# Kernel optimization log

Measured on AMD Instinct MI355X. Metric: run time of the kernel, lower is better.

The kernel has to match this reference:

```python
import jax, jax.numpy as jnp
import numpy as np


def setup_inputs() -> dict:
    key = jax.random.key(0)
    ks = jax.random.split(key, 8)
    b, l, d_model = 2, 2048, 1024
    d_inner, d_state, dt_rank, d_conv = 2048, 16, 64, 4
    g = lambda k, shape, s: jax.random.normal(k, shape, jnp.float32) * s
    A = jnp.broadcast_to(jnp.arange(1, d_state + 1, dtype=jnp.float32), (d_inner, d_state))
    return {
        "x": g(ks[0], (b, l, d_model), 1.0),
        "W_in": g(ks[1], (d_model, 2 * d_inner), 0.02),
        "W_conv": g(ks[2], (d_inner, 1, d_conv), 0.1),
        "b_conv": g(ks[3], (d_inner,), 0.1),
        "W_x": g(ks[4], (d_inner, dt_rank + 2 * d_state), 0.02),
        "W_dt": g(ks[5], (dt_rank, d_inner), 0.02),
        "b_dt": g(ks[6], (d_inner,), 0.1),
        "A_log": jnp.log(A),
        "D": jnp.ones((d_inner,), jnp.float32),
        "W_out": g(ks[7], (d_inner, d_model), 0.02),
    }


def _selective_scan(x, delta, A, B, C, D):
    # x, delta: (b, l, d); A: (d, n); B, C: (b, l, n); D: (d,)
    b, l, d = x.shape
    n = A.shape[1]

    def step(h, inp):
        dt, Bt, Ct, xt = inp  # (b,d), (b,n), (b,n), (b,d)
        dA = jnp.exp(dt[:, :, None] * A)                     # (b,d,n)
        h = dA * h + (dt * xt)[:, :, None] * Bt[:, None, :]  # (b,d,n)
        y = jnp.einsum('bdn,bn->bd', h, Ct)
        return h, y

    h0 = jnp.zeros((b, d, n), x.dtype)
    xs = (jnp.swapaxes(delta, 0, 1), jnp.swapaxes(B, 0, 1),
          jnp.swapaxes(C, 0, 1), jnp.swapaxes(x, 0, 1))
    _, ys = jax.lax.scan(step, h0, xs)   # ys: (l, b, d)
    return jnp.swapaxes(ys, 0, 1) + D * x


def _mamba(x, W_in, W_conv, b_conv, W_x, W_dt, b_dt, A_log, D, W_out):
    b, l, _ = x.shape
    d_inner = W_conv.shape[0]
    d_conv = W_conv.shape[2]
    dt_rank = W_dt.shape[0]
    n = A_log.shape[1]

    xr = x @ W_in                                   # (b,l,2*d_inner)
    xin, res = xr[..., :d_inner], xr[..., d_inner:]

    # depthwise causal conv1d (left pad d_conv-1 == torch pad both + trim to l)
    xc = jnp.swapaxes(xin, 1, 2)                    # (b,d_inner,l)
    xc = jax.lax.conv_general_dilated(
        xc, W_conv, window_strides=(1,), padding=[(d_conv - 1, 0)],
        feature_group_count=d_inner,
        dimension_numbers=('NCH', 'OIH', 'NCH')) + b_conv[None, :, None]
    xs = jax.nn.silu(jnp.swapaxes(xc, 1, 2))        # (b,l,d_inner)

    x_dbl = xs @ W_x                                # (b,l,dt_rank+2n)
    delta = jax.nn.softplus(x_dbl[..., :dt_rank] @ W_dt + b_dt)
    Bm = x_dbl[..., dt_rank:dt_rank + n]
    Cm = x_dbl[..., dt_rank + n:]
    A = -jnp.exp(A_log)

    y = _selective_scan(xs, delta, A, Bm, Cm, D)
    y = y * jax.nn.silu(res)
    return y @ W_out


def reference(x, W_in, W_conv, b_conv, W_x, W_dt, b_dt, A_log, D, W_out):
    return _mamba(x, W_in, W_conv, b_conv, W_x, W_dt, b_dt, A_log, D, W_out)
```

## Files before the change

### kernel.cpp

```cpp
#include <hip/hip_runtime.h>


typedef unsigned short ushort_t;
using short8 = __attribute__((ext_vector_type(8))) short;
using f32x4  = __attribute__((ext_vector_type(4))) float;
using gptr_t = const __attribute__((address_space(1))) unsigned short*;
using sptr_t = __attribute__((address_space(3))) unsigned short*;

#define NC 64
#define CL 32

__device__ inline ushort_t f2bf(float v) {
    unsigned u = __float_as_uint(v);
    unsigned r = (u + 0x7fff + ((u >> 16) & 1)) >> 16;
    return (ushort_t)r;
}
__device__ inline float bf2f(ushort_t h) { return __uint_as_float(((unsigned)h) << 16); }
__device__ inline void split2(float v, ushort_t& h, ushort_t& l) {
    h = f2bf(v);
    l = f2bf(v - bf2f(h));
}

__global__ __launch_bounds__(256) void convert_all(
    const float* __restrict__ x, ushort_t* __restrict__ xh, ushort_t* __restrict__ xl,
    const float* __restrict__ W_in, ushort_t* __restrict__ winh, ushort_t* __restrict__ winl,
    const float* __restrict__ W_out, ushort_t* __restrict__ wouth, ushort_t* __restrict__ woutl,
    const float* __restrict__ W_x, ushort_t* __restrict__ wxh, ushort_t* __restrict__ wxl) {
    __shared__ float tile[32][33];
    const int id = blockIdx.x;
    if (id < 4096) {
        int i = id * 256 + threadIdx.x;
        float4 v = ((const float4*)x)[i];
        ushort4 hh, ll;
        split2(v.x, hh.x, ll.x); split2(v.y, hh.y, ll.y);
        split2(v.z, hh.z, ll.z); split2(v.w, hh.w, ll.w);
        ((ushort4*)xh)[i] = hh;
        ((ushort4*)xl)[i] = ll;
        return;
    }
    const float* W; ushort_t *Th, *Tl; int K, N, bx, by;
    if (id < 8192)       { W = W_in;  Th = winh;  Tl = winl;  K = 1024; N = 4096;
                           bx = (id - 4096) & 127; by = (id - 4096) >> 7; }
    else if (id < 10240) { W = W_out; Th = wouth; Tl = woutl; K = 2048; N = 1024;
                           bx = (id - 8192) & 31;  by = (id - 8192) >> 5; }
    else                 { W = W_x;   Th = wxh;   Tl = wxl;   K = 2048; N = 96;
                           bx = (id - 10240) & 3;  by = (id - 10240) >> 2; }
    int n0 = bx * 32, k0 = by * 32;
    int tx = threadIdx.x & 31, ty = threadIdx.x >> 5;
    #pragma unroll
    for (int j = 0; j < 4; ++j) {
        int k = ty + j * 8;
        tile[k][tx] = (n0 + tx < N) ? W[(size_t)(k0 + k) * N + n0 + tx] : 0.f;
    }
    __syncthreads();
    #pragma unroll
    for (int j = 0; j < 4; ++j) {
        int nrow = ty + j * 8;
        float v = tile[tx][nrow];
        ushort_t h, l;
        split2(v, h, l);
        size_t o = (size_t)(n0 + nrow) * K + k0 + tx;
        Th[o] = h; Tl[o] = l;
    }
}

__global__ __launch_bounds__(512, 2) void gemm_mfma3_256(
    const ushort_t* __restrict__ Ah, const ushort_t* __restrict__ Al,
    const ushort_t* __restrict__ Bh, const ushort_t* __restrict__ Bl,
    float* __restrict__ C, int M, int N, int K, int ksteps, int partial_stride) {
    __shared__ ushort_t lds[65536];
    const int tid  = threadIdx.x;
    const int w    = tid >> 6;
    const int lane = tid & 63;
    const int wr = w >> 2;
    const int wc = w & 3;
    const int fr = lane & 15;
    const int kq = (lane >> 4) * 8;
    const int bm = blockIdx.y * 256;
    const int bn = blockIdx.x * 256;
    const int NT = ksteps;
    const int kbeg = blockIdx.z * ksteps * 32;
    C += (size_t)blockIdx.z * partial_stride;

    const int sg   = tid ^ ((tid >> 3) & 7);
    const int srow = sg >> 2;
    const int skof = (sg & 3) * 8;

    f32x4 acc[8][4];
    #pragma unroll
    for (int i = 0; i < 8; ++i)
        #pragma unroll
        for (int j = 0; j < 4; ++j) acc[i][j] = (f32x4){0.f, 0.f, 0.f, 0.f};

    #define STAGE(t, db)                                                          \
    {                                                                             \
        const int k0_ = kbeg + (t) * 32;                                          \
        _Pragma("unroll")                                                         \
        for (int h_ = 0; h_ < 2; ++h_) {                                          \
            const size_t ga_ = (size_t)(bm + h_ * 128 + srow) * K + k0_ + skof;   \
            const size_t gb_ = (size_t)(bn + h_ * 128 + srow) * K + k0_ + skof;   \
            const int dst_ = (db) * 8192 + h_ * 4096 + w * 512;                   \
            __builtin_amdgcn_global_load_lds((gptr_t)(Ah + ga_), (sptr_t)&lds[0     + dst_], 16, 0, 0); \
            __builtin_amdgcn_global_load_lds((gptr_t)(Al + ga_), (sptr_t)&lds[16384 + dst_], 16, 0, 0); \
            __builtin_amdgcn_global_load_lds((gptr_t)(Bh + gb_), (sptr_t)&lds[32768 + dst_], 16, 0, 0); \
            __builtin_amdgcn_global_load_lds((gptr_t)(Bl + gb_), (sptr_t)&lds[49152 + dst_], 16, 0, 0); \
        }                                                                         \
    }

    #define LDF(arrOff, db, row) \
        (*(const short8*)&lds[(arrOff) + (db) * 8192 + \
            ((((row) << 2) | (kq >> 3)) ^ (((row) >> 1) & 7)) * 8])

    STAGE(0, 0);
    STAGE(1, 1);
    asm volatile("s_waitcnt vmcnt(8)" ::: "memory");
    __builtin_amdgcn_s_barrier();

    for (int t = 0; t < NT; ++t) {
        const int db = t & 1;
        short8 bhF[4], blF[4], ahF[4], alF[4];
        #pragma unroll
        for (int j = 0; j < 4; ++j) {
            const int rowb = wc * 64 + j * 16 + fr;
            bhF[j] = LDF(32768, db, rowb);
            blF[j] = LDF(49152, db, rowb);
        }
        #pragma unroll
        for (int i = 0; i < 4; ++i) {
            const int rowa = wr * 128 + i * 16 + fr;
            ahF[i] = LDF(0, db, rowa);
            alF[i] = LDF(16384, db, rowa);
        }
        __builtin_amdgcn_s_setprio(1);
        #pragma unroll
        for (int i = 0; i < 4; ++i)
            #pragma unroll
            for (int j = 0; j < 4; ++j) {
                acc[i][j] = __builtin_amdgcn_mfma_f32_16x16x32_bf16(ahF[i], bhF[j], acc[i][j], 0, 0, 0);
                acc[i][j] = __builtin_amdgcn_mfma_f32_16x16x32_bf16(ahF[i], blF[j], acc[i][j], 0, 0, 0);
                acc[i][j] = __builtin_amdgcn_mfma_f32_16x16x32_bf16(alF[i], bhF[j], acc[i][j], 0, 0, 0);
            }
        __builtin_amdgcn_s_setprio(0);
        short8 ah2[4], al2[4];
        #pragma unroll
        for (int i = 0; i < 4; ++i) {
            const int rowa = wr * 128 + (i + 4) * 16 + fr;
            ah2[i] = LDF(0, db, rowa);
            al2[i] = LDF(16384, db, rowa);
        }
        asm volatile("s_waitcnt lgkmcnt(0)" ::: "memory");
        __builtin_amdgcn_sched_barrier(0);
        __builtin_amdgcn_s_barrier();
        if (t + 2 < NT) STAGE(t + 2, db);
        __builtin_amdgcn_s_setprio(1);
        #pragma unroll
        for (int i = 0; i < 4; ++i)
            #pragma unroll
            for (int j = 0; j < 4; ++j) {
                acc[i + 4][j] = __builtin_amdgcn_mfma_f32_16x16x32_bf16(ah2[i], bhF[j], acc[i + 4][j], 0, 0, 0);
                acc[i + 4][j] = __builtin_amdgcn_mfma_f32_16x16x32_bf16(ah2[i], blF[j], acc[i + 4][j], 0, 0, 0);
                acc[i + 4][j] = __builtin_amdgcn_mfma_f32_16x16x32_bf16(al2[i], bhF[j], acc[i + 4][j], 0, 0, 0);
            }
        __builtin_amdgcn_s_setprio(0);
        if (t + 2 < NT) {
            asm volatile("s_waitcnt vmcnt(8)" ::: "memory");
        } else {
            asm volatile("s_waitcnt vmcnt(0)" ::: "memory");
        }
        __builtin_amdgcn_sched_barrier(0);
        __builtin_amdgcn_s_barrier();
    }
    #undef STAGE
    #undef LDF

    #pragma unroll
    for (int i = 0; i < 8; ++i) {
        const int row = bm + wr * 128 + i * 16 + (lane >> 4) * 4;
        #pragma unroll
        for (int j = 0; j < 4; ++j) {
            const int col = bn + wc * 64 + j * 16 + fr;
            float* cp = C + (size_t)row * N + col;
            #pragma unroll
            for (int r = 0; r < 4; ++r) cp[(size_t)r * N] = acc[i][j][r];
        }
    }
}

__global__ void reduce4(const float4* __restrict__ p, float4* __restrict__ outp) {
    int i = blockIdx.x * 256 + threadIdx.x;
    float4 s = p[i];
    #pragma unroll
    for (int k = 1; k < 4; ++k) {
        float4 v = p[i + (size_t)k * 1048576];
        s.x += v.x; s.y += v.y; s.z += v.z; s.w += v.w;
    }
    outp[i] = s;
}

__global__ __launch_bounds__(256) void gemm_mfma3_sk(
    const ushort_t* __restrict__ Ah, const ushort_t* __restrict__ Al,
    const ushort_t* __restrict__ Bh, const ushort_t* __restrict__ Bl,
    float* __restrict__ partial, int K) {
    __shared__ ushort_t sAh[4096], sAl[4096], sBh[4096], sBl[4096];
    const int tid  = threadIdx.x;
    const int wid  = tid >> 6;
    const int lane = tid & 63;
    const int kslice = blockIdx.x;
    const int bm = blockIdx.y * 128;
    const int wr = wid >> 1, wc = wid & 1;
    const int kbeg = kslice * 128;

    f32x4 acc[4][4];
    #pragma unroll
    for (int i = 0; i < 4; ++i)
        #pragma unroll
        for (int j = 0; j < 4; ++j) acc[i][j] = (f32x4){0.f, 0.f, 0.f, 0.f};

    for (int k0 = kbeg; k0 < kbeg + 128; k0 += 32) {
        #pragma unroll
        for (int issue = 0; issue < 2; ++issue) {
            const int off = wid * 2048 + issue * 1024 + lane * 16;
            const int row = off >> 6;
            const int ce  = (off & 63) >> 1;
            const size_t ga = (size_t)(bm + row) * K + k0 + ce;
            const size_t gb = (size_t)row * K + k0 + ce;
            const int lo = (wid * 2048 + issue * 1024) >> 1;
            __builtin_amdgcn_global_load_lds((gptr_t)(Ah + ga), (sptr_t)&sAh[lo], 16, 0, 0);
            __builtin_amdgcn_global_load_lds((gptr_t)(Al + ga), (sptr_t)&sAl[lo], 16, 0, 0);
            __builtin_amdgcn_global_load_lds((gptr_t)(Bh + gb), (sptr_t)&sBh[lo], 16, 0, 0);
            __builtin_amdgcn_global_load_lds((gptr_t)(Bl + gb), (sptr_t)&sBl[lo], 16, 0, 0);
        }
        __syncthreads();

        const int fr = lane & 15;
        const int kb = (lane >> 4) * 8;
        short8 ah[4], al[4], bh[4], bl[4];
        #pragma unroll
        for (int i = 0; i < 4; ++i) {
            const int ra = (wr * 64 + i * 16 + fr) * 32 + kb;
            ah[i] = *(const short8*)&sAh[ra];
            al[i] = *(const short8*)&sAl[ra];
            const int rb = (wc * 64 + i * 16 + fr) * 32 + kb;
            bh[i] = *(const short8*)&sBh[rb];
            bl[i] = *(const short8*)&sBl[rb];
        }
        #pragma unroll
        for (int i = 0; i < 4; ++i)
            #pragma unroll
            for (int j = 0; j < 4; ++j) {
                acc[i][j] = __builtin_amdgcn_mfma_f32_16x16x32_bf16(ah[i], bh[j], acc[i][j], 0, 0, 0);
                acc[i][j] = __builtin_amdgcn_mfma_f32_16x16x32_bf16(ah[i], bl[j], acc[i][j], 0, 0, 0);
                acc[i][j] = __builtin_amdgcn_mfma_f32_16x16x32_bf16(al[i], bh[j], acc[i][j], 0, 0, 0);
            }
        __syncthreads();
    }

    float* Cp = partial + (size_t)kslice * 4096 * 96;
    #pragma unroll
    for (int i = 0; i < 4; ++i) {
        int row = bm + wr * 64 + i * 16 + (lane >> 4) * 4;
        #pragma unroll
        for (int j = 0; j < 4; ++j) {
            int col = wc * 64 + j * 16 + (lane & 15);
            if (col < 96) {
                float* cp = Cp + (size_t)row * 96 + col;
                #pragma unroll
                for (int r = 0; r < 4; ++r) cp[(size_t)r * 96] = acc[i][j][r];
            }
        }
    }
}

__global__ __launch_bounds__(256) void reduce_delta(
    const float4* __restrict__ p,
    float* __restrict__ xdbl,
    const float* __restrict__ W_dt,
    const float* __restrict__ b_dt,
    float* __restrict__ delta) {
    __shared__ float rows[16][96];
    const int r0 = blockIdx.x * 16;
    for (int j = threadIdx.x; j < 384; j += 256) {
        int row = j / 24, c4 = j % 24;
        size_t idx = (size_t)(r0 + row) * 24 + c4;
        float4 s = p[idx];
        #pragma unroll
        for (int k = 1; k < 16; ++k) {
            float4 v = p[idx + (size_t)k * 98304];
            s.x += v.x; s.y += v.y; s.z += v.z; s.w += v.w;
        }
        *(float4*)&rows[row][c4 * 4] = s;
        if (c4 >= 16)
            ((float4*)(xdbl + (size_t)(r0 + row) * 128))[c4] = s;
    }
    __syncthreads();
    const int c = threadIdx.x * 8;
    float acc[16][8];
    #pragma unroll
    for (int r = 0; r < 16; ++r)
        #pragma unroll
        for (int j = 0; j < 8; ++j) acc[r][j] = 0.f;
    for (int k = 0; k < 64; ++k) {
        float4 w0 = *(const float4*)&W_dt[(size_t)k * 2048 + c];
        float4 w1 = *(const float4*)&W_dt[(size_t)k * 2048 + c + 4];
        float wv[8] = {w0.x, w0.y, w0.z, w0.w, w1.x, w1.y, w1.z, w1.w};
        #pragma unroll
        for (int r = 0; r < 16; ++r) {
            float dv = rows[r][k];
            #pragma unroll
            for (int j = 0; j < 8; ++j) acc[r][j] = fmaf(dv, wv[j], acc[r][j]);
        }
    }
    float4 b0 = *(const float4*)&b_dt[c];
    float4 b1 = *(const float4*)&b_dt[c + 4];
    float bv[8] = {b0.x, b0.y, b0.z, b0.w, b1.x, b1.y, b1.z, b1.w};
    #pragma unroll
    for (int r = 0; r < 16; ++r) {
        float o[8];
        #pragma unroll
        for (int j = 0; j < 8; ++j) {
            float v = acc[r][j] + bv[j];
            o[j] = (v > 20.f) ? v : log1pf(__expf(v));
        }
        float* dp = delta + (size_t)(r0 + r) * 2048 + c;
        *(float4*)dp       = make_float4(o[0], o[1], o[2], o[3]);
        *(float4*)(dp + 4) = make_float4(o[4], o[5], o[6], o[7]);
    }
}

__global__ void conv_silu_k(const float* __restrict__ xr, const float* __restrict__ Wc,
                            const float* __restrict__ bc,
                            ushort_t* __restrict__ xsh, ushort_t* __restrict__ xsl,
                            int total) {
    for (int idx = blockIdx.x * blockDim.x + threadIdx.x; idx < total;
         idx += gridDim.x * blockDim.x) {
        int d = idx & 2047;
        int l = (idx >> 11) & 2047;
        int b = idx >> 22;
        float acc = bc[d];
        const float* wp = Wc + d * 4;
        #pragma unroll
        for (int k = 0; k < 4; ++k) {
            int ll = l - 3 + k;
            if (ll >= 0)
                acc = fmaf(xr[((size_t)(b * 2048 + ll) << 12) + d], wp[k], acc);
        }
        float v = acc / (1.f + __expf(-acc));
        ushort_t h, lo;
        split2(v, h, lo);
        xsh[idx] = h;
        xsl[idx] = lo;
    }
}

__global__ __launch_bounds__(256) void scan_p1(
    const float* __restrict__ delta,
    const ushort_t* __restrict__ xsh, const ushort_t* __restrict__ xsl,
    const float* __restrict__ xdbl, const float* __restrict__ A_log,
    float* __restrict__ S, float* __restrict__ sumdt) {
    const int u = blockIdx.x * 256 + threadIdx.x;
    const int chunk = u >> 12;
    const int c = u & 4095;
    const int b = c >> 11, d = c & 2047;

    float a[16];
    #pragma unroll
    for (int i = 0; i < 4; ++i) {
        float4 v = ((const float4*)(A_log + d * 16))[i];
        a[4 * i + 0] = -__expf(v.x); a[4 * i + 1] = -__expf(v.y);
        a[4 * i + 2] = -__expf(v.z); a[4 * i + 3] = -__expf(v.w);
    }
    float h[16];
    #pragma unroll
    for (int n = 0; n < 16; ++n) h[n] = 0.f;
    float sdt = 0.f;

    const size_t row0 = (size_t)b * 2048 + (size_t)chunk * CL;
    const float4* xd4 = (const float4*)xdbl;
    #pragma unroll 2
    for (int t = 0; t < CL; ++t) {
        const size_t row = row0 + t;
        float dt = delta[row * 2048 + d];
        float xv = bf2f(xsh[row * 2048 + d]) + bf2f(xsl[row * 2048 + d]);
        float4 Bv[4];
        #pragma unroll
        for (int i = 0; i < 4; ++i) Bv[i] = xd4[row * 32 + 16 + i];
        const float* Bf = (const float*)Bv;
        sdt += dt;
        float du = dt * xv;
        #pragma unroll
        for (int n = 0; n < 16; ++n) {
            float dA = __expf(dt * a[n]);
            h[n] = fmaf(dA, h[n], du * Bf[n]);
        }
    }
    float4* S4 = (float4*)(S + ((size_t)chunk * 4096 + c) * 16);
    #pragma unroll
    for (int i = 0; i < 4; ++i)
        S4[i] = make_float4(h[4 * i + 0], h[4 * i + 1], h[4 * i + 2], h[4 * i + 3]);
    sumdt[chunk * 4096 + c] = sdt;
}

__global__ __launch_bounds__(256) void scan_p2(
    float* __restrict__ S, const float* __restrict__ sumdt,
    const float* __restrict__ A_log) {
    const int idx = blockIdx.x * blockDim.x + threadIdx.x;
    const int n = idx & 15;
    const int c = (idx >> 4) & 4095;
    const int d = c & 2047;
    const float a = -__expf(A_log[d * 16 + n]);
    float h = 0.f;
    for (int k = 0; k < NC; ++k) {
        const size_t o = ((size_t)k * 4096 + c) * 16 + n;
        float carry = S[o];
        S[o] = h;
        float P = __expf(a * sumdt[k * 4096 + c]);
        h = fmaf(P, h, carry);
    }
}

__global__ __launch_bounds__(256) void scan_p3(
    const float* __restrict__ delta,
    const ushort_t* __restrict__ xsh, const ushort_t* __restrict__ xsl,
    const float* __restrict__ xdbl, const float* __restrict__ xr,
    const float* __restrict__ A_log, const float* __restrict__ Dp,
    const float* __restrict__ H0,
    ushort_t* __restrict__ yh, ushort_t* __restrict__ yl) {
    const int u = blockIdx.x * 256 + threadIdx.x;
    const int chunk = u >> 12;
    const int c = u & 4095;
    const int b = c >> 11, d = c & 2047;

    float a[16];
    #pragma unroll
    for (int i = 0; i < 4; ++i) {
        float4 v = ((const float4*)(A_log + d * 16))[i];
        a[4 * i + 0] = -__expf(v.x); a[4 * i + 1] = -__expf(v.y);
        a[4 * i + 2] = -__expf(v.z); a[4 * i + 3] = -__expf(v.w);
    }
    float h[16];
    const float4* H4 = (const float4*)(H0 + ((size_t)chunk * 4096 + c) * 16);
    #pragma unroll
    for (int i = 0; i < 4; ++i) {
        float4 v = H4[i];
        h[4 * i + 0] = v.x; h[4 * i + 1] = v.y; h[4 * i + 2] = v.z; h[4 * i + 3] = v.w;
    }
    const float Dd = Dp[d];

    const size_t row0 = (size_t)b * 2048 + (size_t)chunk * CL;
    const float4* xd4 = (const float4*)xdbl;
    #pragma unroll 2
    for (int t = 0; t < CL; ++t) {
        const size_t row = row0 + t;
        float dt = delta[row * 2048 + d];
        float xv = bf2f(xsh[row * 2048 + d]) + bf2f(xsl[row * 2048 + d]);
        float4 BC[8];
        #pragma unroll
        for (int i = 0; i < 8; ++i) BC[i] = xd4[row * 32 + 16 + i];
        const float* Bf = (const float*)BC;
        const float* Cf = Bf + 16;
        float du = dt * xv;
        float acc = 0.f;
        #pragma unroll
        for (int n = 0; n < 16; ++n) {
            float dA = __expf(dt * a[n]);
            h[n] = fmaf(dA, h[n], du * Bf[n]);
            acc = fmaf(h[n], Cf[n], acc);
        }
        float rv = xr[(row << 12) + 2048 + d];
        float yv = fmaf(Dd, xv, acc) * (rv / (1.f + __expf(-rv)));
        ushort_t hb, lb;
        split2(yv, hb, lb);
        yh[row * 2048 + d] = hb;
        yl[row * 2048 + d] = lb;
    }
}

extern "C" void kernel_launch(void* const* d_in, const int* in_sizes, int n_in,
                              void* d_out, int out_size, void* d_ws, size_t ws_size,
                              hipStream_t stream) {
    const float* x      = (const float*)d_in[0];
    const float* W_in   = (const float*)d_in[1];
    const float* W_conv = (const float*)d_in[2];
    const float* b_conv = (const float*)d_in[3];
    const float* W_x    = (const float*)d_in[4];
    const float* W_dt   = (const float*)d_in[5];
    const float* b_dt   = (const float*)d_in[6];
    const float* A_log  = (const float*)d_in[7];
    const float* Dp     = (const float*)d_in[8];
    const float* W_out  = (const float*)d_in[9];
    float* out = (float*)d_out;

    float* ws    = (float*)d_ws;
    float* xr    = ws;
    float* xdbl  = xr + 16777216;
    float* delta = xdbl + 524288;
    float* S     = delta + 8388608;
    float* sumdt = S + 4194304;
    ushort_t* base = (ushort_t*)(sumdt + 262144);
    ushort_t* xh = base, *xl = base + 4194304;
    ushort_t* winh = base + 8388608, *winl = base + 12582912;
    float*    partial = (float*)base;
    ushort_t* yh = base, *yl = base + 8388608;
    ushort_t* wouth = base + 16777216, *woutl = base + 18874368;
    ushort_t* wxh   = base + 20971520, *wxl   = base + 21233664;
    ushort_t* xsh   = base + 22282240, *xsl   = base + 30670848;
    float* outPartial = xr;

    dim3 blk(256);

    convert_all<<<dim3(10496), blk, 0, stream>>>(x, xh, xl, W_in, winh, winl,
                                                 W_out, wouth, woutl, W_x, wxh, wxl);

    gemm_mfma3_256<<<dim3(16, 16, 1), dim3(512), 0, stream>>>(
        xh, xl, winh, winl, xr, 4096, 4096, 1024, 32, 0);
    conv_silu_k<<<dim3(4096), blk, 0, stream>>>(xr, W_conv, b_conv, xsh, xsl, 8388608);
    gemm_mfma3_sk<<<dim3(16, 32), blk, 0, stream>>>(xsh, xsl, wxh, wxl, partial, 2048);
    reduce_delta<<<dim3(256), blk, 0, stream>>>((const float4*)partial, xdbl,
                                                W_dt, b_dt, delta);
    scan_p1<<<dim3(1024), blk, 0, stream>>>(delta, xsh, xsl, xdbl, A_log, S, sumdt);
    scan_p2<<<dim3(256), blk, 0, stream>>>(S, sumdt, A_log);
    scan_p3<<<dim3(1024), blk, 0, stream>>>(delta, xsh, xsl, xdbl, xr, A_log, Dp, S, yh, yl);
    gemm_mfma3_256<<<dim3(4, 16, 4), dim3(512), 0, stream>>>(
        yh, yl, wouth, woutl, outPartial, 4096, 1024, 2048, 16, 4194304);
    reduce4<<<dim3(4096), blk, 0, stream>>>((const float4*)outPartial, (float4*)out);
}
```

Measured before the change: 544.2 us.

## Replace split-K output GEMM and reduction with a 128x64-tile direct GEMM

The output projection (4096x1024x2048) previously ran as a split-K 256x256-tile GEMM with a 4-way partial buffer followed by a separate reduce kernel. It now uses a new 128x64-tile, 256-thread MFMA kernel with 512 blocks that writes the output directly. This removes the partial-sum writes and reads and one kernel launch. The trade-off is a simple single-buffered loop with a barrier each k-step, no LDS swizzle and less data reuse per block.

After: 552.1 us. About the same (+1.5%).

```diff
diff --git a/kernel.cpp b/kernel.cpp
--- a/kernel.cpp
+++ b/kernel.cpp
@@ -67,7 +67,7 @@
 __global__ __launch_bounds__(512, 2) void gemm_mfma3_256(
     const ushort_t* __restrict__ Ah, const ushort_t* __restrict__ Al,
     const ushort_t* __restrict__ Bh, const ushort_t* __restrict__ Bl,
-    float* __restrict__ C, int M, int N, int K, int ksteps, int partial_stride) {
+    float* __restrict__ C, int M, int N, int K, int ksteps) {
     __shared__ ushort_t lds[65536];
     const int tid  = threadIdx.x;
     const int w    = tid >> 6;
@@ -79,8 +79,6 @@
     const int bm = blockIdx.y * 256;
     const int bn = blockIdx.x * 256;
     const int NT = ksteps;
-    const int kbeg = blockIdx.z * ksteps * 32;
-    C += (size_t)blockIdx.z * partial_stride;
 
     const int sg   = tid ^ ((tid >> 3) & 7);
     const int srow = sg >> 2;
@@ -94,7 +92,7 @@
 
     #define STAGE(t, db)                                                          \
     {                                                                             \
-        const int k0_ = kbeg + (t) * 32;                                          \
+        const int k0_ = (t) * 32;                                                 \
         _Pragma("unroll")                                                         \
         for (int h_ = 0; h_ < 2; ++h_) {                                          \
             const size_t ga_ = (size_t)(bm + h_ * 128 + srow) * K + k0_ + skof;   \
@@ -186,15 +184,83 @@
     }
 }
 
-__global__ void reduce4(const float4* __restrict__ p, float4* __restrict__ outp) {
-    int i = blockIdx.x * 256 + threadIdx.x;
-    float4 s = p[i];
-    #pragma unroll
-    for (int k = 1; k < 4; ++k) {
-        float4 v = p[i + (size_t)k * 1048576];
-        s.x += v.x; s.y += v.y; s.z += v.z; s.w += v.w;
-    }
-    outp[i] = s;
+__global__ __launch_bounds__(256) void gemm_mfma3_n64(
+    const ushort_t* __restrict__ Ah, const ushort_t* __restrict__ Al,
+    const ushort_t* __restrict__ Bh, const ushort_t* __restrict__ Bl,
+    float* __restrict__ C, int M, int N, int K) {
+    __shared__ ushort_t sAh[4096], sAl[4096], sBh[2048], sBl[2048];
+    const int tid  = threadIdx.x;
+    const int wid  = tid >> 6;
+    const int lane = tid & 63;
+    const int bm = blockIdx.y * 128;
+    const int bn = blockIdx.x * 64;
+    const int wr = wid >> 1, wc = wid & 1;
+
+    f32x4 acc[4][2];
+    #pragma unroll
+    for (int i = 0; i < 4; ++i)
+        #pragma unroll
+        for (int j = 0; j < 2; ++j) acc[i][j] = (f32x4){0.f, 0.f, 0.f, 0.f};
+
+    for (int k0 = 0; k0 < K; k0 += 32) {
+        #pragma unroll
+        for (int issue = 0; issue < 2; ++issue) {
+            const int off = issue * 4096 + tid * 16;
+            const int row = off >> 6;
+            const int ce  = (off & 63) >> 1;
+            const size_t ga = (size_t)(bm + row) * K + k0 + ce;
+            const int lo = (issue * 4096 + wid * 1024) >> 1;
+            __builtin_amdgcn_global_load_lds((gptr_t)(Ah + ga), (sptr_t)&sAh[lo], 16, 0, 0);
+            __builtin_amdgcn_global_load_lds((gptr_t)(Al + ga), (sptr_t)&sAl[lo], 16, 0, 0);
+        }
+        {
+            const int off = tid * 16;
+            const int row = off >> 6;
+            const int ce  = (off & 63) >> 1;
+            const size_t gb = (size_t)(bn + row) * K + k0 + ce;
+            const int lo = (wid * 1024) >> 1;
+            __builtin_amdgcn_global_load_lds((gptr_t)(Bh + gb), (sptr_t)&sBh[lo], 16, 0, 0);
+            __builtin_amdgcn_global_load_lds((gptr_t)(Bl + gb), (sptr_t)&sBl[lo], 16, 0, 0);
+        }
+        __syncthreads();
+
+        const int fr = lane & 15;
+        const int kb = (lane >> 4) * 8;
+        short8 ah[4], al[4], bh[2], bl[2];
+        #pragma unroll
+        for (int i = 0; i < 4; ++i) {
+            const int ra = (wr * 64 + i * 16 + fr) * 32 + kb;
+            ah[i] = *(const short8*)&sAh[ra];
+            al[i] = *(const short8*)&sAl[ra];
+        }
+        #pragma unroll
+        for (int j = 0; j < 2; ++j) {
+            const int rb = (wc * 32 + j * 16 + fr) * 32 + kb;
+            bh[j] = *(const short8*)&sBh[rb];
+            bl[j] = *(const short8*)&sBl[rb];
+        }
+        #pragma unroll
+        for (int i = 0; i < 4; ++i)
+            #pragma unroll
+            for (int j = 0; j < 2; ++j) {
+                acc[i][j] = __builtin_amdgcn_mfma_f32_16x16x32_bf16(ah[i], bh[j], acc[i][j], 0, 0, 0);
+                acc[i][j] = __builtin_amdgcn_mfma_f32_16x16x32_bf16(ah[i], bl[j], acc[i][j], 0, 0, 0);
+                acc[i][j] = __builtin_amdgcn_mfma_f32_16x16x32_bf16(al[i], bh[j], acc[i][j], 0, 0, 0);
+            }
+        __syncthreads();
+    }
+
+    #pragma unroll
+    for (int i = 0; i < 4; ++i) {
+        int row = bm + wr * 64 + i * 16 + (lane >> 4) * 4;
+        #pragma unroll
+        for (int j = 0; j < 2; ++j) {
+            int col = bn + wc * 32 + j * 16 + (lane & 15);
+            float* cp = C + (size_t)row * N + col;
+            #pragma unroll
+            for (int r = 0; r < 4; ++r) cp[(size_t)r * N] = acc[i][j][r];
+        }
+    }
 }
 
 __global__ __launch_bounds__(256) void gemm_mfma3_sk(
@@ -504,15 +570,14 @@
     ushort_t* wouth = base + 16777216, *woutl = base + 18874368;
     ushort_t* wxh   = base + 20971520, *wxl   = base + 21233664;
     ushort_t* xsh   = base + 22282240, *xsl   = base + 30670848;
-    float* outPartial = xr;
 
     dim3 blk(256);
 
     convert_all<<<dim3(10496), blk, 0, stream>>>(x, xh, xl, W_in, winh, winl,
                                                  W_out, wouth, woutl, W_x, wxh, wxl);
 
-    gemm_mfma3_256<<<dim3(16, 16, 1), dim3(512), 0, stream>>>(
-        xh, xl, winh, winl, xr, 4096, 4096, 1024, 32, 0);
+    gemm_mfma3_256<<<dim3(16, 16), dim3(512), 0, stream>>>(
+        xh, xl, winh, winl, xr, 4096, 4096, 1024, 32);
     conv_silu_k<<<dim3(4096), blk, 0, stream>>>(xr, W_conv, b_conv, xsh, xsl, 8388608);
     gemm_mfma3_sk<<<dim3(16, 32), blk, 0, stream>>>(xsh, xsl, wxh, wxl, partial, 2048);
     reduce_delta<<<dim3(256), blk, 0, stream>>>((const float4*)partial, xdbl,
@@ -520,7 +585,6 @@
     scan_p1<<<dim3(1024), blk, 0, stream>>>(delta, xsh, xsl, xdbl, A_log, S, sumdt);
     scan_p2<<<dim3(256), blk, 0, stream>>>(S, sumdt, A_log);
     scan_p3<<<dim3(1024), blk, 0, stream>>>(delta, xsh, xsl, xdbl, xr, A_log, Dp, S, yh, yl);
-    gemm_mfma3_256<<<dim3(4, 16, 4), dim3(512), 0, stream>>>(
-        yh, yl, wouth, woutl, outPartial, 4096, 1024, 2048, 16, 4194304);
-    reduce4<<<dim3(4096), blk, 0, stream>>>((const float4*)outPartial, (float4*)out);
-}
+    gemm_mfma3_n64<<<dim3(16, 32), blk, 0, stream>>>(yh, yl, wouth, woutl, out,
+                                                     4096, 1024, 2048);
+}
```
